# Optimization experiments

Hardware: AMD Instinct MI355X
Metric: run time of the kernel (lower is better)

Reference implementation:

```python
import jax, jax.numpy as jnp
import numpy as np

NUM_HEADS = 16


def setup_inputs() -> dict:
    key0 = jax.random.key(0)
    ks = jax.random.split(key0, 8)
    L, S, N, E = 2048, 2048, 2, 1024
    H = NUM_HEADS
    scale = 1.0 / np.sqrt(E)
    return {
        "query": jax.random.normal(ks[0], (L, N, E), jnp.float32),
        "key": jax.random.normal(ks[1], (S, N, E), jnp.float32),
        "value": jax.random.normal(ks[2], (S, N, E), jnp.float32),
        "attn_bias": jax.random.normal(ks[3], (N * H, L, S), jnp.float32) * 0.1,
        "in_proj_weight": jax.random.normal(ks[4], (3 * E, E), jnp.float32) * scale,
        "in_proj_bias": jax.random.normal(ks[5], (3 * E,), jnp.float32) * 0.02,
        "out_proj_weight": jax.random.normal(ks[6], (E, E), jnp.float32) * scale,
        "out_proj_bias": jax.random.normal(ks[7], (E,), jnp.float32) * 0.02,
    }


def reference(query, key, value, attn_bias, in_proj_weight, in_proj_bias,
              out_proj_weight, out_proj_bias):
    # query: (L,N,E); key/value: (S,N,E); attn_bias: (N*H,L,S)
    L, N, E = query.shape
    S = key.shape[0]
    H = NUM_HEADS
    hd = E // H
    scale_factor = 1
    scaling = float(hd * scale_factor) ** (-0.5)

    Wq, Wk, Wv = jnp.split(in_proj_weight, 3, axis=0)
    bq, bk, bv = jnp.split(in_proj_bias, 3)

    q = (query @ Wq.T + bq) * scaling           # (L,N,E)
    k = key @ Wk.T + bk                         # (S,N,E)
    v = value @ Wv.T + bv                       # (S,N,E)

    def to_heads(x):
        T = x.shape[0]
        return x.reshape(T, N, H, hd).transpose(1, 2, 0, 3)  # (N,H,T,hd)

    qh, kh, vh = to_heads(q), to_heads(k), to_heads(v)

    scores = jnp.einsum('nhld,nhsd->nhls', qh, kh) + attn_bias.reshape(N, H, L, S)
    attn = jax.nn.softmax(scores, axis=-1)      # (N,H,L,S)
    out = jnp.einsum('nhls,nhsd->nhld', attn, vh)  # (N,H,L,hd)
    out = out.transpose(2, 0, 1, 3).reshape(L, N, E)  # (L,N,E)
    return out @ out_proj_weight.T + out_proj_bias
```

## Files before the change

kernel.cpp:

```cpp
#include <hip/hip_runtime.h>
#include <hip/hip_bf16.h>
#include <stdint.h>

typedef short bf16x8 __attribute__((ext_vector_type(8)));
typedef float f32x4 __attribute__((ext_vector_type(4)));

__device__ __forceinline__ ushort f2bf(float f) {
  uint x = __float_as_uint(f);
  x += 0x7FFFu + ((x >> 16) & 1u);
  return (ushort)(x >> 16);
}

__device__ __forceinline__ uint cvt_pk_bf16(float lo, float hi) {
  uint r;
  asm("v_cvt_pk_bf16_f32 %0, %1, %2" : "=v"(r) : "v"(lo), "v"(hi));
  return r;
}

__device__ __forceinline__ void gl_lds16(const void* g, void* l) {
  __builtin_amdgcn_global_load_lds(
      (const __attribute__((address_space(1))) unsigned int*)g,
      (__attribute__((address_space(3))) unsigned int*)l, 16, 0, 0);
}

__global__ void __launch_bounds__(256) convert_bf16(
    const float* q, const float* k, const float* v,
    const float* ipw, const float* opw, ushort* dst) {
  size_t e = ((size_t)blockIdx.x * 256 + threadIdx.x) * 8;
  const float* src;
  if (e < 4194304u)        src = q   + e;
  else if (e < 8388608u)   src = k   + (e - 4194304u);
  else if (e < 12582912u)  src = v   + (e - 8388608u);
  else if (e < 15728640u)  src = ipw + (e - 12582912u);
  else                     src = opw + (e - 15728640u);
  float4 a = ((const float4*)src)[0];
  float4 b = ((const float4*)src)[1];
  uint4 o;
  o.x = cvt_pk_bf16(a.x, a.y);
  o.y = cvt_pk_bf16(a.z, a.w);
  o.z = cvt_pk_bf16(b.x, b.y);
  o.w = cvt_pk_bf16(b.z, b.w);
  *(uint4*)(dst + e) = o;
}

__global__ void __launch_bounds__(256) gemm_bf16(
    const ushort* Abase, const ushort* W, const float* bias,
    ushort* oq, ushort* ok, ushort* ov, float* fout, int mode) {
  const int z = blockIdx.z;
  const ushort* A = Abase + (size_t)z * 4194304;
  const int rt = blockIdx.y, ct = blockIdx.x;
  const int tid = threadIdx.x, lane = tid & 63, wid = tid >> 6;
  const int g = lane >> 4, c = lane & 15;
  const int wr = wid >> 1, wc = wid & 1;

  __shared__ ushort Al[2][16 * 512];
  __shared__ ushort Bl[2][16 * 512];

  f32x4 acc[4][4];
#pragma unroll
  for (int i = 0; i < 4; i++)
#pragma unroll
    for (int j = 0; j < 4; j++) acc[i][j] = (f32x4){0.f, 0.f, 0.f, 0.f};

  auto stage = [&](int b, int k0) {
#pragma unroll
    for (int q2 = 0; q2 < 4; q2++) {
      int f = wid * 4 + q2;
      int fr = f >> 3, fm = (f >> 1) & 3, fk = f & 1;
      const ushort* asrc = A + (size_t)(rt * 128 + fr * 64 + fm * 16 + c) * 1024
                             + k0 + fk * 32 + g * 8;
      gl_lds16(asrc, (void*)&Al[b][f * 512]);
      const ushort* bsrc = W + (size_t)(z * 1024 + ct * 128 + fr * 64 + fm * 16 + c) * 1024
                             + k0 + fk * 32 + g * 8;
      gl_lds16(bsrc, (void*)&Bl[b][f * 512]);
    }
  };

  auto compute = [&](int b) {
#pragma unroll
    for (int kk = 0; kk < 2; kk++) {
      bf16x8 af[4], bfr[4];
#pragma unroll
      for (int mi = 0; mi < 4; mi++)
        af[mi] = *(const bf16x8*)&Al[b][(wr * 8 + mi * 2 + kk) * 512 + lane * 8];
#pragma unroll
      for (int ni = 0; ni < 4; ni++)
        bfr[ni] = *(const bf16x8*)&Bl[b][(wc * 8 + ni * 2 + kk) * 512 + lane * 8];
#pragma unroll
      for (int mi = 0; mi < 4; mi++)
#pragma unroll
        for (int ni = 0; ni < 4; ni++)
          acc[mi][ni] = __builtin_amdgcn_mfma_f32_16x16x32_bf16(af[mi], bfr[ni], acc[mi][ni], 0, 0, 0);
    }
  };

  stage(0, 0);
#pragma unroll 1
  for (int kt = 0; kt < 16; kt += 2) {
    __syncthreads();
    if (kt + 1 < 16) stage(1, (kt + 1) * 64);
    compute(0);
    __syncthreads();
    if (kt + 2 < 16) stage(0, (kt + 2) * 64);
    compute(1);
  }

  float bcol[4];
#pragma unroll
  for (int ni = 0; ni < 4; ni++)
    bcol[ni] = bias[z * 1024 + ct * 128 + wc * 64 + ni * 16 + c];

  if (mode == 0) {
    ushort* dst = (z == 0) ? oq : ((z == 1) ? ok : ov);
    float scl = (z == 0) ? 0.125f : 1.0f;
#pragma unroll
    for (int mi = 0; mi < 4; mi++)
#pragma unroll
      for (int r = 0; r < 4; r++) {
        int row = rt * 128 + wr * 64 + mi * 16 + g * 4 + r;
        int t = row >> 1, n = row & 1;
#pragma unroll
        for (int ni = 0; ni < 4; ni++) {
          int col = ct * 128 + wc * 64 + ni * 16 + c;
          int h = col >> 6, d = col & 63;
          float val = (acc[mi][ni][r] + bcol[ni]) * scl;
          dst[((size_t)(n * 16 + h) * 2048 + t) * 64 + d] = f2bf(val);
        }
      }
  } else {
#pragma unroll
    for (int mi = 0; mi < 4; mi++)
#pragma unroll
      for (int r = 0; r < 4; r++) {
        int row = rt * 128 + wr * 64 + mi * 16 + g * 4 + r;
#pragma unroll
        for (int ni = 0; ni < 4; ni++) {
          int col = ct * 128 + wc * 64 + ni * 16 + c;
          fout[(size_t)row * 1024 + col] = acc[mi][ni][r] + bcol[ni];
        }
      }
  }
}

__global__ void __launch_bounds__(256) transpose_v(const ushort* vh, ushort* vhT) {
  const int stile = blockIdx.x, nh = blockIdx.y;
  const int tid = threadIdx.x;
  __shared__ ushort T[64 * 72];
  {
    int s_loc = tid >> 2, dchunk = (tid & 3) * 16;
    const ushort* src = vh + ((size_t)nh * 2048 + stile * 64 + s_loc) * 64 + dchunk;
    union { uint4 u4[2]; ushort us[16]; } u;
    u.u4[0] = *(const uint4*)src;
    u.u4[1] = *(const uint4*)(src + 8);
#pragma unroll
    for (int j = 0; j < 16; j++) T[(dchunk + j) * 72 + s_loc] = u.us[j];
  }
  __syncthreads();
  {
    int d = tid >> 2, schunk = (tid & 3) * 16;
    uint4 o0 = *(const uint4*)&T[d * 72 + schunk];
    uint4 o1 = *(const uint4*)&T[d * 72 + schunk + 8];
    ushort* dst = vhT + ((size_t)nh * 64 + d) * 2048 + stile * 64 + schunk;
    *(uint4*)dst = o0;
    *(uint4*)(dst + 8) = o1;
  }
}

__global__ void __launch_bounds__(256) flash_attn(
    const ushort* qh, const ushort* kh, const ushort* vhT,
    const float* bias, ushort* attnO) {
  const int qt = blockIdx.x, nh = blockIdx.y;
  const int tid = threadIdx.x, lane = tid & 63, w = tid >> 6;
  const int g = lane >> 4, c = lane & 15;
  const int l = qt * 64 + w * 16 + c;
  const int n = nh >> 4, h = nh & 15;

  const ushort* q_nh = qh + (size_t)nh * 2048 * 64;
  const ushort* k_nh = kh + (size_t)nh * 2048 * 64;
  const ushort* v_nh = vhT + (size_t)nh * 64 * 2048;
  const float4* b4 = (const float4*)(bias + (size_t)nh * 2048 * 2048);

  __shared__ ushort Kl[2][8 * 512];
  __shared__ ushort Vl[2][8 * 512];

  bf16x8 qf[2];
#pragma unroll
  for (int kk = 0; kk < 2; kk++)
    qf[kk] = *(const bf16x8*)(q_nh + (size_t)l * 64 + kk * 32 + g * 8);

  f32x4 Oa[4];
#pragma unroll
  for (int ni = 0; ni < 4; ni++) Oa[ni] = (f32x4){0.f, 0.f, 0.f, 0.f};
  float m_run = -1e30f, l_run = 0.f;

  auto stage = [&](int b, int t) {
    int s0 = t * 64;
#pragma unroll
    for (int q2 = 0; q2 < 2; q2++) {
      int f = w + q2 * 4;
      const ushort* ks = k_nh + (size_t)(s0 + (f & 3) * 16 + c) * 64 + (f >> 2) * 32 + g * 8;
      gl_lds16(ks, (void*)&Kl[b][f * 512]);
      const ushort* vs = v_nh + (size_t)((f & 3) * 16 + c) * 2048 + s0 + (f >> 2) * 32 + g * 8;
      gl_lds16(vs, (void*)&Vl[b][f * 512]);
    }
  };

  auto loadbias = [&](float4* bb, int t) {
#pragma unroll
    for (int mi = 0; mi < 4; mi++)
      bb[mi] = b4[(size_t)l * 512 + t * 16 + mi * 4 + g];
  };

  auto compute = [&](int b, const float4* bb) {
    f32x4 sc[4];
#pragma unroll
    for (int mi = 0; mi < 4; mi++)
      sc[mi] = (f32x4){bb[mi].x, bb[mi].y, bb[mi].z, bb[mi].w};
#pragma unroll
    for (int kk = 0; kk < 2; kk++)
#pragma unroll
      for (int mi = 0; mi < 4; mi++) {
        bf16x8 kf = *(const bf16x8*)&Kl[b][(kk * 4 + mi) * 512 + lane * 8];
        sc[mi] = __builtin_amdgcn_mfma_f32_16x16x32_bf16(kf, qf[kk], sc[mi], 0, 0, 0);
      }
    float mx = -1e30f;
#pragma unroll
    for (int mi = 0; mi < 4; mi++)
#pragma unroll
      for (int r = 0; r < 4; r++) mx = fmaxf(mx, sc[mi][r]);
    mx = fmaxf(mx, __shfl_xor(mx, 16, 64));
    mx = fmaxf(mx, __shfl_xor(mx, 32, 64));
    float m_new = fmaxf(m_run, mx);
    const float L2E = 1.4426950408889634f;
    float corr = __builtin_amdgcn_exp2f((m_run - m_new) * L2E);
    float psum = 0.f;
#pragma unroll
    for (int mi = 0; mi < 4; mi++)
#pragma unroll
      for (int r = 0; r < 4; r++) {
        float p = __builtin_amdgcn_exp2f((sc[mi][r] - m_new) * L2E);
        sc[mi][r] = p;
        psum += p;
      }
    psum += __shfl_xor(psum, 16, 64);
    psum += __shfl_xor(psum, 32, 64);
    l_run = l_run * corr + psum;
    m_run = m_new;
#pragma unroll
    for (int ni = 0; ni < 4; ni++) Oa[ni] *= corr;

    uint pk[4][2];
#pragma unroll
    for (int mi = 0; mi < 4; mi++) {
      pk[mi][0] = cvt_pk_bf16(sc[mi][0], sc[mi][1]);
      pk[mi][1] = cvt_pk_bf16(sc[mi][2], sc[mi][3]);
    }
    const int sgb = ((g & 1) * 2) * 16 + c;
    const bool hi = (g >= 2);
#pragma unroll
    for (int kks = 0; kks < 2; kks++) {
      uint dw[4];
#pragma unroll
      for (int j = 0; j < 4; j++) {
        int src = sgb + (j >> 1) * 16;
        uint a0 = (uint)__shfl((int)pk[2 * kks + 0][j & 1], src, 64);
        uint a1 = (uint)__shfl((int)pk[2 * kks + 1][j & 1], src, 64);
        dw[j] = hi ? a1 : a0;
      }
      union { uint u[4]; bf16x8 v; } pb;
      pb.u[0] = dw[0]; pb.u[1] = dw[1]; pb.u[2] = dw[2]; pb.u[3] = dw[3];
#pragma unroll
      for (int ni = 0; ni < 4; ni++) {
        bf16x8 vf = *(const bf16x8*)&Vl[b][(kks * 4 + ni) * 512 + lane * 8];
        Oa[ni] = __builtin_amdgcn_mfma_f32_16x16x32_bf16(vf, pb.v, Oa[ni], 0, 0, 0);
      }
    }
  };

  float4 biasA[4], biasB[4];
  stage(0, 0);
  loadbias(biasA, 0);
#pragma unroll 1
  for (int t = 0; t < 32; t += 2) {
    __syncthreads();
    if (t + 1 < 32) { stage(1, t + 1); loadbias(biasB, t + 1); }
    compute(0, biasA);
    __syncthreads();
    if (t + 2 < 32) { stage(0, t + 2); loadbias(biasA, t + 2); }
    compute(1, biasB);
  }

  float inv = 1.0f / l_run;
  size_t obase = ((size_t)(l * 2 + n)) * 1024 + h * 64;
#pragma unroll
  for (int ni = 0; ni < 4; ni++) {
    ushort4 o;
    o.x = f2bf(Oa[ni][0] * inv);
    o.y = f2bf(Oa[ni][1] * inv);
    o.z = f2bf(Oa[ni][2] * inv);
    o.w = f2bf(Oa[ni][3] * inv);
    *(ushort4*)(attnO + obase + ni * 16 + g * 4) = o;
  }
}

extern "C" void kernel_launch(void* const* d_in, const int* in_sizes, int n_in,
                              void* d_out, int out_size, void* d_ws, size_t ws_size,
                              hipStream_t stream) {
  (void)in_sizes; (void)n_in; (void)out_size; (void)ws_size;
  const float* query = (const float*)d_in[0];
  const float* key   = (const float*)d_in[1];
  const float* value = (const float*)d_in[2];
  const float* abias = (const float*)d_in[3];
  const float* ipw   = (const float*)d_in[4];
  const float* ipb   = (const float*)d_in[5];
  const float* opw   = (const float*)d_in[6];
  const float* opb   = (const float*)d_in[7];
  float* out = (float*)d_out;

  ushort* ws   = (ushort*)d_ws;
  ushort* Xq   = ws;
  ushort* Wqkv = ws + 12582912;
  ushort* Wo   = ws + 15728640;
  ushort* qh   = ws + 16777216;
  ushort* kh   = ws + 20971520;
  ushort* vh   = ws + 25165824;
  ushort* vhT  = ws;
  ushort* attnO = ws + 4194304;

  convert_bf16<<<8192, 256, 0, stream>>>(query, key, value, ipw, opw, ws);
  gemm_bf16<<<dim3(8, 32, 3), 256, 0, stream>>>(Xq, Wqkv, ipb, qh, kh, vh, nullptr, 0);
  transpose_v<<<dim3(32, 32), 256, 0, stream>>>(vh, vhT);
  flash_attn<<<dim3(32, 32), 256, 0, stream>>>(qh, kh, vhT, abias, attnO);
  gemm_bf16<<<dim3(8, 32, 1), 256, 0, stream>>>(attnO, Wo, opb, nullptr, nullptr, nullptr, out, 1);
}
```

Before: 895.4 us.

## Stage attention bias tiles into swizzled LDS via async global-to-LDS loads

Moves the per-tile attention-bias fetch in the flash-attention kernel off per-lane global float4 register loads. It now uses the same double-buffered async global_load_lds path already used for K and V. Each bias row is read as contiguous 256-byte segments and stored in LDS with an XOR swizzle so the later per-lane float4 reads avoid bank conflicts. This is meant to coalesce the dominant bias traffic and relieve register pressure from the two bias register buffers. In exchange it adds 32 KB of LDS per block, which may lower occupancy.

```diff
diff --git a/kernel.cpp b/kernel.cpp
--- a/kernel.cpp
+++ b/kernel.cpp
@@ -173,15 +173,17 @@
   const int tid = threadIdx.x, lane = tid & 63, w = tid >> 6;
   const int g = lane >> 4, c = lane & 15;
   const int l = qt * 64 + w * 16 + c;
+  const int lloc = w * 16 + c;
   const int n = nh >> 4, h = nh & 15;
 
   const ushort* q_nh = qh + (size_t)nh * 2048 * 64;
   const ushort* k_nh = kh + (size_t)nh * 2048 * 64;
   const ushort* v_nh = vhT + (size_t)nh * 64 * 2048;
-  const float4* b4 = (const float4*)(bias + (size_t)nh * 2048 * 2048);
+  const float* bias_nh = bias + (size_t)nh * 2048 * 2048;
 
   __shared__ ushort Kl[2][8 * 512];
   __shared__ ushort Vl[2][8 * 512];
+  __shared__ float Bi[2][64 * 64];
 
   bf16x8 qf[2];
 #pragma unroll
@@ -203,19 +205,25 @@
       const ushort* vs = v_nh + (size_t)((f & 3) * 16 + c) * 2048 + s0 + (f >> 2) * 32 + g * 8;
       gl_lds16(vs, (void*)&Vl[b][f * 512]);
     }
+#pragma unroll
+    for (int p = 0; p < 4; p++) {
+      int idxb = p * 256 + w * 64;
+      int idx = idxb + lane;
+      int row = idx >> 4;
+      int c4 = (idx & 15) ^ (row & 15);
+      const float* bs = bias_nh + (size_t)(qt * 64 + row) * 2048 + s0 + c4 * 4;
+      gl_lds16(bs, (void*)&Bi[b][idxb * 4]);
+    }
   };
 
-  auto loadbias = [&](float4* bb, int t) {
-#pragma unroll
-    for (int mi = 0; mi < 4; mi++)
-      bb[mi] = b4[(size_t)l * 512 + t * 16 + mi * 4 + g];
-  };
-
-  auto compute = [&](int b, const float4* bb) {
+  auto compute = [&](int b) {
     f32x4 sc[4];
 #pragma unroll
-    for (int mi = 0; mi < 4; mi++)
-      sc[mi] = (f32x4){bb[mi].x, bb[mi].y, bb[mi].z, bb[mi].w};
+    for (int mi = 0; mi < 4; mi++) {
+      int s4 = (mi * 4 + g) ^ (lloc & 15);
+      float4 bb = *(const float4*)&Bi[b][(lloc * 16 + s4) * 4];
+      sc[mi] = (f32x4){bb.x, bb.y, bb.z, bb.w};
+    }
 #pragma unroll
     for (int kk = 0; kk < 2; kk++)
 #pragma unroll
@@ -277,17 +285,15 @@
     }
   };
 
-  float4 biasA[4], biasB[4];
   stage(0, 0);
-  loadbias(biasA, 0);
 #pragma unroll 1
   for (int t = 0; t < 32; t += 2) {
     __syncthreads();
-    if (t + 1 < 32) { stage(1, t + 1); loadbias(biasB, t + 1); }
-    compute(0, biasA);
+    if (t + 1 < 32) stage(1, t + 1);
+    compute(0);
     __syncthreads();
-    if (t + 2 < 32) { stage(0, t + 2); loadbias(biasA, t + 2); }
-    compute(1, biasB);
+    if (t + 2 < 32) stage(0, t + 2);
+    compute(1);
   }
 
   float inv = 1.0f / l_run;
```

Result: no change. 889.2 us (-0.7%).
